# Kernel tuning notes

Hardware: AMD Instinct MI355X
Metric: run time of the kernel (lower is better)

Reference implementation:

```python
import jax, jax.numpy as jnp
import numpy as np

EPS = 1e-12  # torch F.normalize eps
SIGMA_RBF = 1.0  # rbf bandwidth (init arg sigma=1)


def _l2norm(v, axis=-1):
    return v / jnp.maximum(jnp.linalg.norm(v, axis=axis, keepdims=True), EPS)


def setup_inputs() -> dict:
    key = jax.random.key(0)
    kx, kw, kb, ku, kc = jax.random.split(key, 5)
    B, C, E, F = 512, 100, 2048, 128
    x = jax.random.normal(kx, (B, E), dtype=jnp.float32)
    # per-class Linear weights [C, F, E] and biases [C, F] (torch Linear layout: out x in)
    bound = 1.0 / np.sqrt(E)
    W = jax.random.uniform(kw, (C, F, E), minval=-bound, maxval=bound, dtype=jnp.float32)
    b = jax.random.uniform(kb, (C, F), minval=-bound, maxval=bound, dtype=jnp.float32)
    # spectral-norm power-iteration vectors u (one per class, normalized)
    u = _l2norm(jax.random.normal(ku, (C, F), dtype=jnp.float32))
    # centroid buffer c (EMA means; randn stand-in for a trained state)
    c = jax.random.normal(kc, (C, F), dtype=jnp.float32)
    return {"x": x, "W": W, "b": b, "u": u, "c": c}


def reference(x, W, b, u, c):
    # --- spectral norm: one power-iteration step per class (torch default) ---
    v = _l2norm(jnp.einsum('cfe,cf->ce', W, u))        # v = normalize(W^T u)  [C,E]
    u2 = _l2norm(jnp.einsum('cfe,ce->cf', W, v))       # u = normalize(W v)    [C,F]
    sigma = jnp.einsum('cf,cfe,ce->c', u2, W, v)       # sigma = u^T W v       [C]
    Wn = W / sigma[:, None, None]
    # --- fused per-class linear projections: z[b,c,f] ---
    z = jnp.einsum('be,cfe->bcf', x, Wn) + b[None, :, :]
    # --- RBF to centroids: exp(-||c - z||^2 / (2 sigma^2)) ---
    dist2 = jnp.sum((c[None, :, :] - z) ** 2, axis=-1)  # [B, C]
    probs = jnp.exp(-dist2 / (2.0 * SIGMA_RBF ** 2))
    return probs
```

## Files before the change

### kernel.cpp

```cpp
#include <hip/hip_runtime.h>
#include <math.h>

#define B_ 512
#define C_ 100
#define E_ 2048
#define F_ 128

typedef _Float16 f16x8 __attribute__((ext_vector_type(8)));
typedef float    f32x4 __attribute__((ext_vector_type(4)));
typedef float    f32x2 __attribute__((ext_vector_type(2)));

#define AS1q __attribute__((address_space(1)))
#define AS3q __attribute__((address_space(3)))

__device__ __forceinline__ void gl_lds16(const void* g, void* lds_base) {
    __builtin_amdgcn_global_load_lds((const AS1q void*)g, (AS3q void*)lds_base, 16, 0, 0);
}

__device__ __forceinline__ f16x8 frag_ld(const float* T, int r, int p) {
    const int k = r & 15;
    const int b = r << 6;
    const f32x4 lo = *(const f32x4*)&T[b + ((((p << 1))     ^ k) << 2)];
    const f32x4 hi = *(const f32x4*)&T[b + ((((p << 1) | 1) ^ k) << 2)];
    f16x8 fr;
    fr[0] = (_Float16)lo[0]; fr[1] = (_Float16)lo[1];
    fr[2] = (_Float16)lo[2]; fr[3] = (_Float16)lo[3];
    fr[4] = (_Float16)hi[0]; fr[5] = (_Float16)hi[1];
    fr[6] = (_Float16)hi[2]; fr[7] = (_Float16)hi[3];
    return fr;
}

__global__ __launch_bounds__(256, 8)
void k_prep(const float* __restrict__ x, _Float16* __restrict__ xh) {
    const size_t base = (size_t)blockIdx.x * 8192 + (size_t)threadIdx.x * 8;
#pragma unroll
    for (int it = 0; it < 4; ++it) {
        const size_t idx = base + (size_t)it * 2048;
        float4 a  = *(const float4*)(x + idx);
        float4 bb = *(const float4*)(x + idx + 4);
        f16x8 h;
        h[0] = (_Float16)a.x;  h[1] = (_Float16)a.y;  h[2] = (_Float16)a.z;  h[3] = (_Float16)a.w;
        h[4] = (_Float16)bb.x; h[5] = (_Float16)bb.y; h[6] = (_Float16)bb.z; h[7] = (_Float16)bb.w;
        *(f16x8*)(xh + idx) = h;
    }
}

__global__ __launch_bounds__(256, 2)
void k_fused(const float* __restrict__ W, const _Float16* __restrict__ xh,
             const float* __restrict__ bias, const float* __restrict__ cent,
             const float* __restrict__ u, float* __restrict__ out) {
    const int bid  = blockIdx.x;
    const int xcd  = bid & 7;
    const int slot = bid >> 3;
    const int c    = xcd * 13 + (slot >> 2);
    if (c >= C_) return;
    const int b0 = (slot & 3) * 128;

    const int t  = threadIdx.x;
    const int w  = t >> 6;
    const int l  = t & 63;
    const int wm = w & 1, wn = w >> 1;
    const int ln = l & 15, quad = l >> 4;

    __shared__ float    Ts[128 * 64];
    __shared__ _Float16 Xs[128 * 64];
    __shared__ float    vs[64];
    __shared__ float    ys[128];
    __shared__ float    red2[2][2];
    __shared__ float    s_rsig;

    f32x4 acc[4][4];
#pragma unroll
    for (int mt = 0; mt < 4; ++mt)
#pragma unroll
        for (int nt = 0; nt < 4; ++nt) acc[mt][nt] = (f32x4){0.f, 0.f, 0.f, 0.f};
    f32x4 y_acc[4];
#pragma unroll
    for (int nt = 0; nt < 4; ++nt) y_acc[nt] = (f32x4){0.f, 0.f, 0.f, 0.f};

    const int lrow4 = l >> 4, cs = l & 15;
    const float* wbase = W + (size_t)c * F_ * E_;
    const int lr = l >> 3;
    const int lg = (l & 7) ^ lr;
    const _Float16* xsrc = xh + (size_t)(b0 + w * 32 + lr) * E_ + lg * 8;

    const int p_  = t >> 3;
    const int sub = t & 7;
    const int gA  = p_ >> 1;
    const int wiA = (p_ & 1) * 2;
    float ur[16];
#pragma unroll
    for (int j = 0; j < 16; ++j) ur[j] = u[(size_t)c * F_ + sub * 16 + j];

    float bi[4], ce[4];
#pragma unroll
    for (int nt = 0; nt < 4; ++nt) {
        int f = wn * 64 + nt * 16 + ln;
        bi[nt] = bias[c * F_ + f];
        ce[nt] = cent[c * F_ + f];
    }

    for (int k0 = 0; k0 < E_; k0 += 64) {
#pragma unroll
        for (int qq = 0; qq < 8; ++qq) {
            const int q   = w * 8 + qq;
            const int r   = q * 4 + lrow4;
            const int off = ((cs ^ (r & 15)) << 2);
            gl_lds16(wbase + (size_t)r * E_ + k0 + off, &Ts[q * 256]);
        }
#pragma unroll
        for (int q = 0; q < 4; ++q)
            gl_lds16(xsrc + (size_t)q * 8 * E_ + k0, &Xs[(w * 4 + q) * 512]);
        __syncthreads();

        {
            float p0 = 0.f, p1 = 0.f;
#pragma unroll
            for (int j = 0; j < 16; ++j) {
                const int f = sub * 16 + j;
                const f32x2 wv = *(const f32x2*)&Ts[(f << 6) + ((gA ^ (f & 15)) << 2) + wiA];
                p0 = fmaf(wv[0], ur[j], p0);
                p1 = fmaf(wv[1], ur[j], p1);
            }
            p0 += __shfl_xor(p0, 1, 64); p1 += __shfl_xor(p1, 1, 64);
            p0 += __shfl_xor(p0, 2, 64); p1 += __shfl_xor(p1, 2, 64);
            p0 += __shfl_xor(p0, 4, 64); p1 += __shfl_xor(p1, 4, 64);
            if (sub == 0) { vs[2 * p_] = p0; vs[2 * p_ + 1] = p1; }
        }

        f16x8 bv[2][4];
#pragma unroll
        for (int kh = 0; kh < 2; ++kh) {
            const int g0 = kh * 4 + quad;
            const int sw = (g0 ^ (ln & 7)) * 8;
            f16x8 av[4];
#pragma unroll
            for (int mt = 0; mt < 4; ++mt)
                av[mt] = *(const f16x8*)&Xs[(wm * 64 + mt * 16 + ln) * 64 + sw];
#pragma unroll
            for (int nt = 0; nt < 4; ++nt)
                bv[kh][nt] = frag_ld(Ts, wn * 64 + nt * 16 + ln, g0);
#pragma unroll
            for (int mt = 0; mt < 4; ++mt)
#pragma unroll
                for (int nt = 0; nt < 4; ++nt)
                    acc[mt][nt] = __builtin_amdgcn_mfma_f32_16x16x32_f16(
                        av[mt], bv[kh][nt], acc[mt][nt], 0, 0, 0);
        }
        __syncthreads();

#pragma unroll
        for (int kh = 0; kh < 2; ++kh) {
            f16x8 vf;
#pragma unroll
            for (int j = 0; j < 8; ++j) vf[j] = (_Float16)0.0f;
            if (ln == 0) {
                const float* vp = &vs[kh * 32 + quad * 8];
                const f32x4 a  = *(const f32x4*)vp;
                const f32x4 bq = *(const f32x4*)(vp + 4);
                vf[0] = (_Float16)a[0];  vf[1] = (_Float16)a[1];
                vf[2] = (_Float16)a[2];  vf[3] = (_Float16)a[3];
                vf[4] = (_Float16)bq[0]; vf[5] = (_Float16)bq[1];
                vf[6] = (_Float16)bq[2]; vf[7] = (_Float16)bq[3];
            }
#pragma unroll
            for (int nt = 0; nt < 4; ++nt)
                y_acc[nt] = __builtin_amdgcn_mfma_f32_16x16x32_f16(
                    bv[kh][nt], vf, y_acc[nt], 0, 0, 0);
        }
    }

    if (wm == 0 && ln == 0) {
#pragma unroll
        for (int nt = 0; nt < 4; ++nt)
#pragma unroll
            for (int r = 0; r < 4; ++r)
                ys[wn * 64 + nt * 16 + quad * 4 + r] = y_acc[nt][r];
    }
    __syncthreads();
    if (t < 128) {
        float yf  = ys[t];
        float nvp = u[(size_t)c * F_ + t] * yf;
        float tsp = yf * yf;
        for (int off = 32; off; off >>= 1) {
            nvp += __shfl_down(nvp, off, 64);
            tsp += __shfl_down(tsp, off, 64);
        }
        if (l == 0) { red2[w][0] = nvp; red2[w][1] = tsp; }
    }
    __syncthreads();
    if (t == 0) s_rsig = sqrtf((red2[0][0] + red2[1][0]) / (red2[0][1] + red2[1][1]));
    __syncthreads();
    const float rsigma = s_rsig;

    float* red = (float*)&Xs[0];

#pragma unroll
    for (int mt = 0; mt < 4; ++mt) {
#pragma unroll
        for (int r = 0; r < 4; ++r) {
            float part = 0.f;
#pragma unroll
            for (int nt = 0; nt < 4; ++nt) {
                float z = fmaf(acc[mt][nt][r], rsigma, bi[nt]);
                float d = ce[nt] - z;
                part = fmaf(d, d, part);
            }
            part += __shfl_xor(part, 1, 64);
            part += __shfl_xor(part, 2, 64);
            part += __shfl_xor(part, 4, 64);
            part += __shfl_xor(part, 8, 64);
            if (ln == 0) {
                int m = wm * 64 + mt * 16 + quad * 4 + r;
                red[m * 2 + wn] = part;
            }
        }
    }
    __syncthreads();
    if (t < 128) {
        float d2 = red[t * 2] + red[t * 2 + 1];
        out[(size_t)(b0 + t) * C_ + c] = expf(-0.5f * d2);
    }
}

extern "C" void kernel_launch(void* const* d_in, const int* in_sizes, int n_in,
                              void* d_out, int out_size, void* d_ws, size_t ws_size,
                              hipStream_t stream) {
    const float* x  = (const float*)d_in[0];
    const float* W  = (const float*)d_in[1];
    const float* b  = (const float*)d_in[2];
    const float* u  = (const float*)d_in[3];
    const float* cc = (const float*)d_in[4];
    float* out = (float*)d_out;

    _Float16* xh = (_Float16*)d_ws;

    k_prep<<<128, 256, 0, stream>>>(x, xh);
    k_fused<<<416, 256, 0, stream>>>(W, xh, b, cc, u, out);
}
```

Measured before the change: 228.5 us.

## Pre-convert W to fp16 and precompute W^T u in a separate pass

A new pre-pass kernel reads the fp32 W once. It writes an fp16 copy to the workspace, computes v = W^T u per class, and converts x to fp16. The main kernel then streams fp16 W tiles directly into LDS with the same swizzle as x, and reads v from a per-class LDS buffer. This removes the in-loop fp32-to-fp16 fragment conversion, the per-tile v reduction and one barrier per iteration, and halves the LDS tile size, so occupancy can rise to 3 blocks. The cost is an extra pass that writes and re-reads an fp16 W copy in global memory.

```diff
diff --git a/kernel.cpp b/kernel.cpp
--- a/kernel.cpp
+++ b/kernel.cpp
@@ -7,8 +7,8 @@
 #define F_ 128
 
 typedef _Float16 f16x8 __attribute__((ext_vector_type(8)));
+typedef _Float16 f16x2 __attribute__((ext_vector_type(2)));
 typedef float    f32x4 __attribute__((ext_vector_type(4)));
-typedef float    f32x2 __attribute__((ext_vector_type(2)));
 
 #define AS1q __attribute__((address_space(1)))
 #define AS3q __attribute__((address_space(3)))
@@ -17,38 +17,65 @@
     __builtin_amdgcn_global_load_lds((const AS1q void*)g, (AS3q void*)lds_base, 16, 0, 0);
 }
 
-__device__ __forceinline__ f16x8 frag_ld(const float* T, int r, int p) {
-    const int k = r & 15;
-    const int b = r << 6;
-    const f32x4 lo = *(const f32x4*)&T[b + ((((p << 1))     ^ k) << 2)];
-    const f32x4 hi = *(const f32x4*)&T[b + ((((p << 1) | 1) ^ k) << 2)];
-    f16x8 fr;
-    fr[0] = (_Float16)lo[0]; fr[1] = (_Float16)lo[1];
-    fr[2] = (_Float16)lo[2]; fr[3] = (_Float16)lo[3];
-    fr[4] = (_Float16)hi[0]; fr[5] = (_Float16)hi[1];
-    fr[6] = (_Float16)hi[2]; fr[7] = (_Float16)hi[3];
-    return fr;
-}
-
-__global__ __launch_bounds__(256, 8)
-void k_prep(const float* __restrict__ x, _Float16* __restrict__ xh) {
-    const size_t base = (size_t)blockIdx.x * 8192 + (size_t)threadIdx.x * 8;
-#pragma unroll
-    for (int it = 0; it < 4; ++it) {
-        const size_t idx = base + (size_t)it * 2048;
-        float4 a  = *(const float4*)(x + idx);
-        float4 bb = *(const float4*)(x + idx + 4);
-        f16x8 h;
-        h[0] = (_Float16)a.x;  h[1] = (_Float16)a.y;  h[2] = (_Float16)a.z;  h[3] = (_Float16)a.w;
-        h[4] = (_Float16)bb.x; h[5] = (_Float16)bb.y; h[6] = (_Float16)bb.z; h[7] = (_Float16)bb.w;
-        *(f16x8*)(xh + idx) = h;
-    }
-}
-
-__global__ __launch_bounds__(256, 2)
-void k_fused(const float* __restrict__ W, const _Float16* __restrict__ xh,
-             const float* __restrict__ bias, const float* __restrict__ cent,
-             const float* __restrict__ u, float* __restrict__ out) {
+__global__ __launch_bounds__(256, 4)
+void k_conv(const float* __restrict__ W, _Float16* __restrict__ Wh,
+            const float* __restrict__ x, _Float16* __restrict__ xh,
+            const float* __restrict__ u, float* __restrict__ v) {
+    const int b = blockIdx.x;
+    const int t = threadIdx.x;
+
+    if (b >= 400) {
+        const size_t base = (size_t)(b - 400) * 32768 + t * 8;
+#pragma unroll
+        for (int it = 0; it < 16; ++it) {
+            const size_t idx = base + (size_t)it * 2048;
+            float4 a  = *(const float4*)(x + idx);
+            float4 bb = *(const float4*)(x + idx + 4);
+            f16x8 h;
+            h[0] = (_Float16)a.x;  h[1] = (_Float16)a.y;  h[2] = (_Float16)a.z;  h[3] = (_Float16)a.w;
+            h[4] = (_Float16)bb.x; h[5] = (_Float16)bb.y; h[6] = (_Float16)bb.z; h[7] = (_Float16)bb.w;
+            *(f16x8*)(xh + idx) = h;
+        }
+        return;
+    }
+
+    const int c   = b >> 2;
+    const int col = (b & 3) * 512 + (t >> 6) * 128 + (t & 63) * 2;
+
+    const float* wsrc = W  + (size_t)c * F_ * E_ + col;
+    _Float16*    wdst = Wh + (size_t)c * F_ * E_ + col;
+    const float* uc   = u  + (size_t)c * F_;
+
+    float v0 = 0.f, v1 = 0.f;
+
+    for (int r8 = 0; r8 < 16; ++r8) {
+        float2 wv[8];
+        float  ub[8];
+#pragma unroll
+        for (int j = 0; j < 8; ++j) {
+            const int r = r8 * 8 + j;
+            wv[j] = *(const float2*)(wsrc + (size_t)r * E_);
+            ub[j] = uc[r];
+        }
+#pragma unroll
+        for (int j = 0; j < 8; ++j) {
+            const int r = r8 * 8 + j;
+            f16x2 h;
+            h[0] = (_Float16)wv[j].x;
+            h[1] = (_Float16)wv[j].y;
+            *(f16x2*)(wdst + (size_t)r * E_) = h;
+            v0 = fmaf(wv[j].x, ub[j], v0);
+            v1 = fmaf(wv[j].y, ub[j], v1);
+        }
+    }
+    *(float2*)(v + (size_t)c * E_ + col) = (float2){v0, v1};
+}
+
+__global__ __launch_bounds__(256, 3)
+void k_main(const _Float16* __restrict__ xh, const _Float16* __restrict__ Wh,
+            const float* __restrict__ bias, const float* __restrict__ cent,
+            const float* __restrict__ u, const float* __restrict__ v,
+            float* __restrict__ out) {
     const int bid  = blockIdx.x;
     const int xcd  = bid & 7;
     const int slot = bid >> 3;
@@ -62,13 +89,19 @@
     const int wm = w & 1, wn = w >> 1;
     const int ln = l & 15, quad = l >> 4;
 
-    __shared__ float    Ts[128 * 64];
     __shared__ _Float16 Xs[128 * 64];
-    __shared__ float    vs[64];
+    __shared__ _Float16 Ws[128 * 64];
+    __shared__ float    Vs[E_];
     __shared__ float    ys[128];
     __shared__ float    red2[2][2];
     __shared__ float    s_rsig;
 
+    {
+        const float* vsrc = v + (size_t)c * E_;
+        *(f32x4*)&Vs[t * 8]     = *(const f32x4*)&vsrc[t * 8];
+        *(f32x4*)&Vs[t * 8 + 4] = *(const f32x4*)&vsrc[t * 8 + 4];
+    }
+
     f32x4 acc[4][4];
 #pragma unroll
     for (int mt = 0; mt < 4; ++mt)
@@ -78,19 +111,10 @@
 #pragma unroll
     for (int nt = 0; nt < 4; ++nt) y_acc[nt] = (f32x4){0.f, 0.f, 0.f, 0.f};
 
-    const int lrow4 = l >> 4, cs = l & 15;
-    const float* wbase = W + (size_t)c * F_ * E_;
     const int lr = l >> 3;
     const int lg = (l & 7) ^ lr;
     const _Float16* xsrc = xh + (size_t)(b0 + w * 32 + lr) * E_ + lg * 8;
-
-    const int p_  = t >> 3;
-    const int sub = t & 7;
-    const int gA  = p_ >> 1;
-    const int wiA = (p_ & 1) * 2;
-    float ur[16];
-#pragma unroll
-    for (int j = 0; j < 16; ++j) ur[j] = u[(size_t)c * F_ + sub * 16 + j];
+    const _Float16* wsrc = Wh + ((size_t)c * F_ + w * 32 + lr) * E_ + lg * 8;
 
     float bi[4], ce[4];
 #pragma unroll
@@ -102,60 +126,36 @@
 
     for (int k0 = 0; k0 < E_; k0 += 64) {
 #pragma unroll
-        for (int qq = 0; qq < 8; ++qq) {
-            const int q   = w * 8 + qq;
-            const int r   = q * 4 + lrow4;
-            const int off = ((cs ^ (r & 15)) << 2);
-            gl_lds16(wbase + (size_t)r * E_ + k0 + off, &Ts[q * 256]);
-        }
-#pragma unroll
         for (int q = 0; q < 4; ++q)
             gl_lds16(xsrc + (size_t)q * 8 * E_ + k0, &Xs[(w * 4 + q) * 512]);
+#pragma unroll
+        for (int q = 0; q < 4; ++q)
+            gl_lds16(wsrc + (size_t)q * 8 * E_ + k0, &Ws[(w * 4 + q) * 512]);
         __syncthreads();
 
-        {
-            float p0 = 0.f, p1 = 0.f;
-#pragma unroll
-            for (int j = 0; j < 16; ++j) {
-                const int f = sub * 16 + j;
-                const f32x2 wv = *(const f32x2*)&Ts[(f << 6) + ((gA ^ (f & 15)) << 2) + wiA];
-                p0 = fmaf(wv[0], ur[j], p0);
-                p1 = fmaf(wv[1], ur[j], p1);
-            }
-            p0 += __shfl_xor(p0, 1, 64); p1 += __shfl_xor(p1, 1, 64);
-            p0 += __shfl_xor(p0, 2, 64); p1 += __shfl_xor(p1, 2, 64);
-            p0 += __shfl_xor(p0, 4, 64); p1 += __shfl_xor(p1, 4, 64);
-            if (sub == 0) { vs[2 * p_] = p0; vs[2 * p_ + 1] = p1; }
-        }
-
-        f16x8 bv[2][4];
 #pragma unroll
         for (int kh = 0; kh < 2; ++kh) {
-            const int g0 = kh * 4 + quad;
+            const int g0 = (kh << 2) + quad;
             const int sw = (g0 ^ (ln & 7)) * 8;
-            f16x8 av[4];
+            f16x8 av[4], bv[4];
 #pragma unroll
             for (int mt = 0; mt < 4; ++mt)
                 av[mt] = *(const f16x8*)&Xs[(wm * 64 + mt * 16 + ln) * 64 + sw];
 #pragma unroll
             for (int nt = 0; nt < 4; ++nt)
-                bv[kh][nt] = frag_ld(Ts, wn * 64 + nt * 16 + ln, g0);
+                bv[nt] = *(const f16x8*)&Ws[(wn * 64 + nt * 16 + ln) * 64 + sw];
 #pragma unroll
             for (int mt = 0; mt < 4; ++mt)
 #pragma unroll
                 for (int nt = 0; nt < 4; ++nt)
                     acc[mt][nt] = __builtin_amdgcn_mfma_f32_16x16x32_f16(
-                        av[mt], bv[kh][nt], acc[mt][nt], 0, 0, 0);
-        }
-        __syncthreads();
-
-#pragma unroll
-        for (int kh = 0; kh < 2; ++kh) {
+                        av[mt], bv[nt], acc[mt][nt], 0, 0, 0);
+
             f16x8 vf;
 #pragma unroll
             for (int j = 0; j < 8; ++j) vf[j] = (_Float16)0.0f;
             if (ln == 0) {
-                const float* vp = &vs[kh * 32 + quad * 8];
+                const float* vp = &Vs[k0 + kh * 32 + quad * 8];
                 const f32x4 a  = *(const f32x4*)vp;
                 const f32x4 bq = *(const f32x4*)(vp + 4);
                 vf[0] = (_Float16)a[0];  vf[1] = (_Float16)a[1];
@@ -166,8 +166,9 @@
 #pragma unroll
             for (int nt = 0; nt < 4; ++nt)
                 y_acc[nt] = __builtin_amdgcn_mfma_f32_16x16x32_f16(
-                    bv[kh][nt], vf, y_acc[nt], 0, 0, 0);
-        }
+                    bv[nt], vf, y_acc[nt], 0, 0, 0);
+        }
+        __syncthreads();
     }
 
     if (wm == 0 && ln == 0) {
@@ -233,8 +234,12 @@
     const float* cc = (const float*)d_in[4];
     float* out = (float*)d_out;
 
-    _Float16* xh = (_Float16*)d_ws;
-
-    k_prep<<<128, 256, 0, stream>>>(x, xh);
-    k_fused<<<416, 256, 0, stream>>>(W, xh, b, cc, u, out);
-}
+    char* ws = (char*)d_ws;
+    _Float16* Wh = (_Float16*)ws;
+    _Float16* xh = (_Float16*)(ws + (size_t)C_ * F_ * E_ * 2);
+    float*    v  = (float*)(ws + (size_t)C_ * F_ * E_ * 2 + (size_t)B_ * E_ * 2);
+
+    k_conv<<<432, 256, 0, stream>>>(W, Wh, x, xh, u, v);
+
+    k_main<<<416, 256, 0, stream>>>(xh, Wh, b, cc, u, v, out);
+}
```

Measured after the change: 214.9 us. -5.9%, faster.
